# Kernel tuning notes

Measured on AMD Instinct MI355X. Metric: run time of the kernel, lower is better.

Reference implementation:

```python
import jax, jax.numpy as jnp
import numpy as np

B, C_IN, L = 1024, 3, 2048
D, K = 64, 8192          # embedding_dim, num_embeddings
BETA = 0.25
SLOPE = 0.001            # LeakyReLU negative slope


def _leaky(x):
    return jnp.where(x > 0, x, SLOPE * x)


def setup_inputs() -> dict:
    key = jax.random.key(0)
    ks = jax.random.split(key, 16)
    def lin(k, fan_in, shape):  # torch default conv init ~ U(-1/sqrt(fan_in), 1/sqrt(fan_in))
        b = 1.0 / np.sqrt(fan_in)
        return jax.random.uniform(k, shape, jnp.float32, -b, b)
    inp = {
        "x":  jax.random.normal(ks[0], (B, C_IN, L), jnp.float32),
        # encoder conv1x1 weights stored as [out, in]
        "W1": lin(ks[1], C_IN, (64, C_IN)),  "b1": lin(ks[2], C_IN, (64,)),
        "W2": lin(ks[3], 64,   (128, 64)),   "b2": lin(ks[4], 64,  (128,)),
        "W3": lin(ks[5], 128,  (D, 128)),    "b3": lin(ks[6], 128, (D,)),
        # codebook init: uniform(-1/K, 1/K) as in the torch module
        "codebook": jax.random.uniform(ks[7], (K, D), jnp.float32, -1.0 / K, 1.0 / K),
        # decoder convtranspose1x1 weights stored as [in, out]
        "U1": lin(ks[8],  D,   (D, 128)),    "c1": lin(ks[9],  D,   (128,)),
        "U2": lin(ks[10], 128, (128, 64)),   "c2": lin(ks[11], 128, (64,)),
        "U3": lin(ks[12], 64,  (64, C_IN)),  "c3": lin(ks[13], 64,  (C_IN,)),
    }
    return inp


def reference(x, W1, b1, W2, b2, W3, b3, codebook, U1, c1, U2, c2, U3, c3):
    # ---- encoder: conv1x1 stack over [B, C, L] then global max pool ----
    h = _leaky(jnp.einsum('oc,bcl->bol', W1, x) + b1[None, :, None])   # [B,64,L]
    h = _leaky(jnp.einsum('oc,bcl->bol', W2, h) + b2[None, :, None])   # [B,128,L]
    h = jnp.einsum('oc,bcl->bol', W3, h) + b3[None, :, None]           # [B,D,L]
    z = jnp.max(h, axis=-1)                                            # [B,D]

    # ---- vector quantizer ----
    d = (jnp.sum(z * z, axis=1, keepdims=True)
         + jnp.sum(codebook * codebook, axis=1)
         - 2.0 * z @ codebook.T)                                       # [B,K]
    idx = jnp.argmin(d, axis=1)                                        # [B]
    z_q = codebook[idx]                                                # [B,D]
    sg = jax.lax.stop_gradient
    loss = jnp.mean((sg(z_q) - z) ** 2) + BETA * jnp.mean((z_q - sg(z)) ** 2)
    z_q_st = z + sg(z_q - z)                                           # straight-through

    # ---- decoder: convtranspose1x1 on length-1 sequence == dense layers ----
    g = _leaky(z_q_st @ U1 + c1)                                       # [B,128]
    g = _leaky(g @ U2 + c2)                                            # [B,64]
    x_recon = (g @ U3 + c3)[:, :, None]                                # [B,3,1]
    return x_recon, loss, z
```

## Files before the change

kernel.cpp:

```cpp
#include <hip/hip_runtime.h>
#include <hip/hip_bf16.h>

#define BB 1024
#define LL 2048
#define KK 8192

typedef _Float16 f16x8 __attribute__((ext_vector_type(8)));
typedef _Float16 f16x2 __attribute__((ext_vector_type(2)));
typedef float    f32x4 __attribute__((ext_vector_type(4)));

__device__ __forceinline__ float leakyf(float v){ return fmaxf(v, 0.001f*v); }

__global__ __launch_bounds__(256, 2) void encoder_mfma(
    const float* __restrict__ x,
    const float* __restrict__ W1, const float* __restrict__ b1,
    const float* __restrict__ W2, const float* __restrict__ b2,
    const float* __restrict__ W3, const float* __restrict__ b3,
    float* __restrict__ z_out, _Float16* __restrict__ zh_out)
{
    const int b    = blockIdx.x;
    const int t    = threadIdx.x;
    const int wave = t >> 6;
    const int lane = t & 63;
    const int col  = lane & 15;
    const int quad = lane >> 4;

    __shared__ __align__(16) _Float16 h2lds[4*16*136];
    __shared__ float red[4][64];

    f16x8 w2f[2][8];
    #pragma unroll
    for (int ks=0; ks<2; ks++){
        #pragma unroll
        for (int nt=0; nt<8; nt++){
            const float* p = W2 + (nt*16+col)*64 + quad*8 + 32*ks;
            f16x8 f;
            #pragma unroll
            for (int j=0;j<8;j++) f[j] = (_Float16)p[j];
            w2f[ks][nt] = f;
        }
    }
    f16x8 w3f[4][4];
    #pragma unroll
    for (int ks=0; ks<4; ks++){
        #pragma unroll
        for (int nt=0; nt<4; nt++){
            const float* p = W3 + (nt*16+col)*128 + quad*8 + 32*ks;
            f16x8 f;
            #pragma unroll
            for (int j=0;j<8;j++) f[j] = (_Float16)p[j];
            w3f[ks][nt] = f;
        }
    }
    f16x2 w1p[2][4][3];
    f16x2 b1p[2][4];
    #pragma unroll
    for (int ks=0; ks<2; ks++){
        #pragma unroll
        for (int j2=0; j2<4; j2++){
            int c0 = quad*8 + 2*j2 + 32*ks;
            #pragma unroll
            for (int i=0;i<3;i++){
                f16x2 w; w[0] = (_Float16)W1[c0*3+i]; w[1] = (_Float16)W1[(c0+1)*3+i];
                w1p[ks][j2][i] = w;
            }
            f16x2 bb; bb[0] = (_Float16)b1[c0]; bb[1] = (_Float16)b1[c0+1];
            b1p[ks][j2] = bb;
        }
    }
    float bb2[8];
    #pragma unroll
    for (int nt=0; nt<8; nt++) bb2[nt] = b2[nt*16+col];

    f32x4 hm[4];
    #pragma unroll
    for (int nt=0;nt<4;nt++){
        hm[nt][0] = -__builtin_inff(); hm[nt][1] = -__builtin_inff();
        hm[nt][2] = -__builtin_inff(); hm[nt][3] = -__builtin_inff();
    }

    const float* xb = x + (size_t)b*3*LL;
    const int wave_off = wave*16*136;
    const int pbase = wave*16 + col;

    float x0n = xb[pbase], x1n = xb[LL+pbase], x2n = xb[2*LL+pbase];

    #pragma unroll 1
    for (int it=0; it<LL/64; it++){
        const float x0 = x0n, x1 = x1n, x2 = x2n;
        {
            int itn = it+1 < 32 ? it+1 : 31;
            int pn = itn*64 + pbase;
            x0n = xb[pn]; x1n = xb[LL+pn]; x2n = xb[2*LL+pn];
        }
        f16x2 xh0; xh0[0] = (_Float16)x0; xh0[1] = xh0[0];
        f16x2 xh1; xh1[0] = (_Float16)x1; xh1[1] = xh1[0];
        f16x2 xh2; xh2[0] = (_Float16)x2; xh2[1] = xh2[0];

        f16x8 a2[2];
        #pragma unroll
        for (int ks=0; ks<2; ks++){
            f16x8 a;
            #pragma unroll
            for (int j2=0; j2<4; j2++){
                f16x2 v = b1p[ks][j2];
                v += w1p[ks][j2][0]*xh0;
                v += w1p[ks][j2][1]*xh1;
                v += w1p[ks][j2][2]*xh2;
                _Float16 e0 = v[0], e1 = v[1];
                e0 = (e0 > (_Float16)0) ? e0 : e0*(_Float16)0.001f;
                e1 = (e1 > (_Float16)0) ? e1 : e1*(_Float16)0.001f;
                a[2*j2]   = e0;
                a[2*j2+1] = e1;
            }
            a2[ks] = a;
        }

        #pragma unroll
        for (int ph=0; ph<2; ph++){
            f32x4 acc2[4];
            #pragma unroll
            for (int n=0; n<4; n++){
                float bb = bb2[ph*4+n];
                acc2[n][0]=bb; acc2[n][1]=bb; acc2[n][2]=bb; acc2[n][3]=bb;
            }
            #pragma unroll
            for (int n=0; n<4; n++){
                acc2[n] = __builtin_amdgcn_mfma_f32_16x16x32_f16(a2[0], w2f[0][ph*4+n], acc2[n], 0,0,0);
                acc2[n] = __builtin_amdgcn_mfma_f32_16x16x32_f16(a2[1], w2f[1][ph*4+n], acc2[n], 0,0,0);
            }
            #pragma unroll
            for (int n=0; n<4; n++){
                #pragma unroll
                for (int j=0; j<4; j++){
                    float v = leakyf(acc2[n][j]);
                    h2lds[wave_off + (quad*4+j)*136 + (ph*4+n)*16+col] = (_Float16)v;
                }
            }
        }

        f32x4 acc3[4];
        #pragma unroll
        for (int nt=0; nt<4; nt++){ acc3[nt][0]=0.f; acc3[nt][1]=0.f; acc3[nt][2]=0.f; acc3[nt][3]=0.f; }
        #pragma unroll
        for (int ks=0; ks<4; ks++){
            f16x8 a3 = *(const f16x8*)&h2lds[wave_off + col*136 + quad*8 + 32*ks];
            #pragma unroll
            for (int nt=0; nt<4; nt++)
                acc3[nt] = __builtin_amdgcn_mfma_f32_16x16x32_f16(a3, w3f[ks][nt], acc3[nt], 0,0,0);
        }
        #pragma unroll
        for (int nt=0; nt<4; nt++){
            hm[nt][0] = fmaxf(hm[nt][0], acc3[nt][0]);
            hm[nt][1] = fmaxf(hm[nt][1], acc3[nt][1]);
            hm[nt][2] = fmaxf(hm[nt][2], acc3[nt][2]);
            hm[nt][3] = fmaxf(hm[nt][3], acc3[nt][3]);
        }
    }

    #pragma unroll
    for (int nt=0; nt<4; nt++){
        float v = fmaxf(fmaxf(hm[nt][0], hm[nt][1]), fmaxf(hm[nt][2], hm[nt][3]));
        v = fmaxf(v, __shfl_xor(v, 16, 64));
        v = fmaxf(v, __shfl_xor(v, 32, 64));
        if (quad == 0) red[wave][nt*16 + col] = v;
    }
    __syncthreads();
    if (t < 64){
        float v = fmaxf(fmaxf(red[0][t], red[1][t]), fmaxf(red[2][t], red[3][t])) + b3[t];
        z_out[(size_t)b*64 + t] = v;
        zh_out[(size_t)b*64 + t] = (_Float16)v;
    }
}

__global__ __launch_bounds__(256, 4) void vq_prep(
    const float* __restrict__ cb, _Float16* __restrict__ cbh, float* __restrict__ cnorm)
{
    const int t = threadIdx.x;
    const int e = blockIdx.x*4 + (t>>6);
    const int d = t & 63;
    float v = cb[(size_t)e*64 + d];
    cbh[(size_t)e*64 + d] = (_Float16)v;
    float p = v*v;
    #pragma unroll
    for (int s=32;s>0;s>>=1) p += __shfl_xor(p, s, 64);
    if (d==0) cnorm[e] = p;
}

__global__ __launch_bounds__(256, 2) void vq_mfma(
    const _Float16* __restrict__ zh, const _Float16* __restrict__ cbh,
    const float* __restrict__ cnorm,
    float* __restrict__ pval, int* __restrict__ pidx)
{
    const int t    = threadIdx.x;
    const int wave = t >> 6;
    const int lane = t & 63;
    const int col  = lane & 15;
    const int quad = lane >> 4;
    const int rb   = blockIdx.x >> 5;
    const int ns   = blockIdx.x & 31;
    const int rowbase = rb*64 + wave*16;

    f16x8 az[2];
    az[0] = *(const f16x8*)&zh[(size_t)(rowbase+col)*64 + quad*8];
    az[1] = *(const f16x8*)&zh[(size_t)(rowbase+col)*64 + quad*8 + 32];

    float best[4] = {__builtin_inff(),__builtin_inff(),__builtin_inff(),__builtin_inff()};
    int   bidx[4] = {0,0,0,0};

    int e = ns*256;
    f16x8 bf0 = *(const f16x8*)&cbh[(size_t)(e+col)*64 + quad*8];
    f16x8 bf1 = *(const f16x8*)&cbh[(size_t)(e+col)*64 + quad*8 + 32];
    float cn  = cnorm[e+col];

    #pragma unroll 1
    for (int nt=0; nt<16; nt++){
        f16x8 c0 = bf0, c1 = bf1;
        float cnc = cn;
        int ec = e;
        if (nt < 15){
            e += 16;
            bf0 = *(const f16x8*)&cbh[(size_t)(e+col)*64 + quad*8];
            bf1 = *(const f16x8*)&cbh[(size_t)(e+col)*64 + quad*8 + 32];
            cn  = cnorm[e+col];
        }
        f32x4 acc; acc[0]=0.f; acc[1]=0.f; acc[2]=0.f; acc[3]=0.f;
        acc = __builtin_amdgcn_mfma_f32_16x16x32_f16(az[0], c0, acc, 0,0,0);
        acc = __builtin_amdgcn_mfma_f32_16x16x32_f16(az[1], c1, acc, 0,0,0);
        int myidx = ec + col;
        #pragma unroll
        for (int r=0; r<4; r++){
            float d = fmaf(-2.0f, acc[r], cnc);
            if (d < best[r]){ best[r] = d; bidx[r] = myidx; }
        }
    }

    #pragma unroll
    for (int r=0; r<4; r++){
        float v = best[r]; int i = bidx[r];
        #pragma unroll
        for (int s=1; s<16; s<<=1){
            float ov = __shfl_xor(v, s, 64);
            int   oi = __shfl_xor(i, s, 64);
            if (ov < v || (ov == v && oi < i)){ v = ov; i = oi; }
        }
        if (col == 0){
            int row = rowbase + quad*4 + r;
            pval[row*32 + ns] = v;
            pidx[row*32 + ns] = i;
        }
    }
}

__global__ __launch_bounds__(256, 4) void vq_merge(
    const float* __restrict__ pval, const int* __restrict__ pidx, int* __restrict__ idx_out)
{
    const int row = blockIdx.x*256 + threadIdx.x;
    float best = __builtin_inff(); int bi = 0;
    #pragma unroll 4
    for (int s=0; s<32; s++){
        float v = pval[row*32 + s]; int i = pidx[row*32 + s];
        if (v < best || (v == best && i < bi)){ best = v; bi = i; }
    }
    idx_out[row] = bi;
}

__global__ __launch_bounds__(128, 1) void decoder_kernel(
    const float* __restrict__ z, const int* __restrict__ idx,
    const float* __restrict__ cb,
    const float* __restrict__ U1, const float* __restrict__ c1,
    const float* __restrict__ U2, const float* __restrict__ c2,
    const float* __restrict__ U3, const float* __restrict__ c3,
    float* __restrict__ xrec, float* __restrict__ loss_part)
{
    const int b = blockIdx.x;
    const int t = threadIdx.x;
    __shared__ float zst[64];
    __shared__ float g1[128];
    __shared__ float g2[64];
    const int kk = idx[b];
    if (t < 64){
        float zv = z[(size_t)b*64 + t];
        float zq = cb[(size_t)kk*64 + t];
        float diff = zq - zv;
        zst[t] = zv + diff;
        float p = diff*diff;
        #pragma unroll
        for (int s=32;s>0;s>>=1) p += __shfl_xor(p, s, 64);
        if (t==0) loss_part[b] = p;
    }
    __syncthreads();
    {
        float v = c1[t];
        #pragma unroll
        for (int d=0; d<64; d++) v = fmaf(zst[d], U1[d*128+t], v);
        g1[t] = leakyf(v);
    }
    __syncthreads();
    if (t < 64){
        float v = c2[t];
        #pragma unroll
        for (int j=0;j<128;j++) v = fmaf(g1[j], U2[j*64+t], v);
        g2[t] = leakyf(v);
    }
    __syncthreads();
    if (t < 3){
        float v = c3[t];
        #pragma unroll
        for (int j=0;j<64;j++) v = fmaf(g2[j], U3[j*3+t], v);
        xrec[(size_t)b*3 + t] = v;
    }
}

__global__ __launch_bounds__(256, 1) void loss_kernel(
    const float* __restrict__ loss_part, float* __restrict__ out)
{
    const int t = threadIdx.x;
    float s = 0.f;
    for (int i=t;i<BB;i+=256) s += loss_part[i];
    #pragma unroll
    for (int sh=32;sh>0;sh>>=1) s += __shfl_xor(s, sh, 64);
    __shared__ float w[4];
    if ((t&63)==0) w[t>>6] = s;
    __syncthreads();
    if (t==0) out[0] = (w[0]+w[1]+w[2]+w[3]) * (1.25f / 65536.0f);
}

extern "C" void kernel_launch(void* const* d_in, const int* in_sizes, int n_in,
                              void* d_out, int out_size, void* d_ws, size_t ws_size,
                              hipStream_t stream)
{
    const float* x  = (const float*)d_in[0];
    const float* W1 = (const float*)d_in[1];
    const float* b1 = (const float*)d_in[2];
    const float* W2 = (const float*)d_in[3];
    const float* b2 = (const float*)d_in[4];
    const float* W3 = (const float*)d_in[5];
    const float* b3 = (const float*)d_in[6];
    const float* cb = (const float*)d_in[7];
    const float* U1 = (const float*)d_in[8];
    const float* c1 = (const float*)d_in[9];
    const float* U2 = (const float*)d_in[10];
    const float* c2 = (const float*)d_in[11];
    const float* U3 = (const float*)d_in[12];
    const float* c3 = (const float*)d_in[13];

    float* out  = (float*)d_out;
    float* xrec = out;
    float* loss = out + 3072;
    float* z    = out + 3073;

    char* ws = (char*)d_ws;
    int*      idx   = (int*)ws;
    float*    lp    = (float*)(ws + 4096);
    _Float16* zh    = (_Float16*)(ws + 8192);
    float*    cnorm = (float*)(ws + 139264);
    float*    pval  = (float*)(ws + 172032);
    int*      pidx  = (int*)(ws + 303104);
    _Float16* cbh   = (_Float16*)(ws + 434176);

    hipLaunchKernelGGL(encoder_mfma, dim3(BB), dim3(256), 0, stream,
                       x, W1, b1, W2, b2, W3, b3, z, zh);
    hipLaunchKernelGGL(vq_prep, dim3(KK/4), dim3(256), 0, stream, cb, cbh, cnorm);
    hipLaunchKernelGGL(vq_mfma, dim3(512), dim3(256), 0, stream, zh, cbh, cnorm, pval, pidx);
    hipLaunchKernelGGL(vq_merge, dim3(4), dim3(256), 0, stream, pval, pidx, idx);
    hipLaunchKernelGGL(decoder_kernel, dim3(BB), dim3(128), 0, stream,
                       z, idx, cb, U1, c1, U2, c2, U3, c3, xrec, lp);
    hipLaunchKernelGGL(loss_kernel, dim3(1), dim3(256), 0, stream, lp, loss);
}
```

Measured before the change: 247.6 us.

## Fuse VQ merge into decoder, pack-convert encoder epilogue, swizzle LDS, vectorize prep

The encoder's layer-2 epilogue now converts MFMA results to packed fp16 before applying the bias and LeakyReLU, and writes to LDS through an XOR swizzle to cut bank conflicts. The input-layer LeakyReLU uses a packed max instead of per-element selects. vq_prep loads float4 and stores packed half4 with a 16-lane reduction. The separate vq_merge kernel is removed and its argmin is folded into the decoder through a warp shuffle reduction, which saves one launch. Doing the bias and activation in fp16 changes rounding slightly, which could flip a near-tied argmin.

Measured after the change: 226.2 us. 1.09x faster.

```diff
diff --git a/kernel.cpp b/kernel.cpp
--- a/kernel.cpp
+++ b/kernel.cpp
@@ -6,10 +6,14 @@
 #define KK 8192
 
 typedef _Float16 f16x8 __attribute__((ext_vector_type(8)));
+typedef _Float16 f16x4 __attribute__((ext_vector_type(4)));
 typedef _Float16 f16x2 __attribute__((ext_vector_type(2)));
 typedef float    f32x4 __attribute__((ext_vector_type(4)));
 
 __device__ __forceinline__ float leakyf(float v){ return fmaxf(v, 0.001f*v); }
+__device__ __forceinline__ f16x2 pkrtz(float a, float b){
+    return __builtin_bit_cast(f16x2, __builtin_amdgcn_cvt_pkrtz(a, b));
+}
 
 __global__ __launch_bounds__(256, 2) void encoder_mfma(
     const float* __restrict__ x,
@@ -68,9 +72,15 @@
             b1p[ks][j2] = bb;
         }
     }
-    float bb2[8];
-    #pragma unroll
-    for (int nt=0; nt<8; nt++) bb2[nt] = b2[nt*16+col];
+    f16x2 b2p[8];
+    #pragma unroll
+    for (int nt=0; nt<8; nt++){
+        _Float16 bv = (_Float16)b2[nt*16+col];
+        f16x2 p; p[0]=bv; p[1]=bv; b2p[nt]=p;
+    }
+
+    f16x2 k001; k001[0] = (_Float16)0.001f; k001[1] = (_Float16)0.001f;
+    f32x4 zc; zc[0]=0.f; zc[1]=0.f; zc[2]=0.f; zc[3]=0.f;
 
     f32x4 hm[4];
     #pragma unroll
@@ -80,8 +90,9 @@
     }
 
     const float* xb = x + (size_t)b*3*LL;
-    const int wave_off = wave*16*136;
+    const int wave_off = wave*2176;
     const int pbase = wave*16 + col;
+    const int rswz  = (col >> 2) << 4;
 
     float x0n = xb[pbase], x1n = xb[LL+pbase], x2n = xb[2*LL+pbase];
 
@@ -107,54 +118,47 @@
                 v += w1p[ks][j2][0]*xh0;
                 v += w1p[ks][j2][1]*xh1;
                 v += w1p[ks][j2][2]*xh2;
-                _Float16 e0 = v[0], e1 = v[1];
-                e0 = (e0 > (_Float16)0) ? e0 : e0*(_Float16)0.001f;
-                e1 = (e1 > (_Float16)0) ? e1 : e1*(_Float16)0.001f;
-                a[2*j2]   = e0;
-                a[2*j2+1] = e1;
+                v = __builtin_elementwise_max(v, v*k001);
+                a[2*j2]   = v[0];
+                a[2*j2+1] = v[1];
             }
             a2[ks] = a;
         }
 
         #pragma unroll
         for (int ph=0; ph<2; ph++){
-            f32x4 acc2[4];
             #pragma unroll
             for (int n=0; n<4; n++){
-                float bb = bb2[ph*4+n];
-                acc2[n][0]=bb; acc2[n][1]=bb; acc2[n][2]=bb; acc2[n][3]=bb;
+                const int nt = ph*4 + n;
+                f32x4 acc = __builtin_amdgcn_mfma_f32_16x16x32_f16(a2[0], w2f[0][nt], zc, 0,0,0);
+                acc = __builtin_amdgcn_mfma_f32_16x16x32_f16(a2[1], w2f[1][nt], acc, 0,0,0);
+                f16x2 p01 = pkrtz(acc[0], acc[1]);
+                f16x2 p23 = pkrtz(acc[2], acc[3]);
+                p01 += b2p[nt];  p23 += b2p[nt];
+                p01 = __builtin_elementwise_max(p01, p01*k001);
+                p23 = __builtin_elementwise_max(p23, p23*k001);
+                _Float16* wp = &h2lds[wave_off + quad*4*136 + ((nt ^ quad)<<4) + col];
+                wp[0]     = p01[0];
+                wp[136]   = p01[1];
+                wp[272]   = p23[0];
+                wp[408]   = p23[1];
             }
-            #pragma unroll
-            for (int n=0; n<4; n++){
-                acc2[n] = __builtin_amdgcn_mfma_f32_16x16x32_f16(a2[0], w2f[0][ph*4+n], acc2[n], 0,0,0);
-                acc2[n] = __builtin_amdgcn_mfma_f32_16x16x32_f16(a2[1], w2f[1][ph*4+n], acc2[n], 0,0,0);
-            }
-            #pragma unroll
-            for (int n=0; n<4; n++){
-                #pragma unroll
-                for (int j=0; j<4; j++){
-                    float v = leakyf(acc2[n][j]);
-                    h2lds[wave_off + (quad*4+j)*136 + (ph*4+n)*16+col] = (_Float16)v;
-                }
-            }
-        }
-
-        f32x4 acc3[4];
-        #pragma unroll
-        for (int nt=0; nt<4; nt++){ acc3[nt][0]=0.f; acc3[nt][1]=0.f; acc3[nt][2]=0.f; acc3[nt][3]=0.f; }
-        #pragma unroll
-        for (int ks=0; ks<4; ks++){
-            f16x8 a3 = *(const f16x8*)&h2lds[wave_off + col*136 + quad*8 + 32*ks];
-            #pragma unroll
-            for (int nt=0; nt<4; nt++)
-                acc3[nt] = __builtin_amdgcn_mfma_f32_16x16x32_f16(a3, w3f[ks][nt], acc3[nt], 0,0,0);
-        }
+        }
+
+        f16x8 a30 = *(const f16x8*)&h2lds[wave_off + col*136 + (( 0 + quad*8) ^ rswz)];
+        f16x8 a31 = *(const f16x8*)&h2lds[wave_off + col*136 + ((32 + quad*8) ^ rswz)];
+        f16x8 a32 = *(const f16x8*)&h2lds[wave_off + col*136 + ((64 + quad*8) ^ rswz)];
+        f16x8 a33 = *(const f16x8*)&h2lds[wave_off + col*136 + ((96 + quad*8) ^ rswz)];
         #pragma unroll
         for (int nt=0; nt<4; nt++){
-            hm[nt][0] = fmaxf(hm[nt][0], acc3[nt][0]);
-            hm[nt][1] = fmaxf(hm[nt][1], acc3[nt][1]);
-            hm[nt][2] = fmaxf(hm[nt][2], acc3[nt][2]);
-            hm[nt][3] = fmaxf(hm[nt][3], acc3[nt][3]);
+            f32x4 acc = __builtin_amdgcn_mfma_f32_16x16x32_f16(a30, w3f[0][nt], zc, 0,0,0);
+            acc = __builtin_amdgcn_mfma_f32_16x16x32_f16(a31, w3f[1][nt], acc, 0,0,0);
+            acc = __builtin_amdgcn_mfma_f32_16x16x32_f16(a32, w3f[2][nt], acc, 0,0,0);
+            acc = __builtin_amdgcn_mfma_f32_16x16x32_f16(a33, w3f[3][nt], acc, 0,0,0);
+            hm[nt][0] = fmaxf(hm[nt][0], acc[0]);
+            hm[nt][1] = fmaxf(hm[nt][1], acc[1]);
+            hm[nt][2] = fmaxf(hm[nt][2], acc[2]);
+            hm[nt][3] = fmaxf(hm[nt][3], acc[3]);
         }
     }
 
@@ -173,18 +177,22 @@
     }
 }
 
-__global__ __launch_bounds__(256, 4) void vq_prep(
+__global__ __launch_bounds__(256, 2) void vq_prep(
     const float* __restrict__ cb, _Float16* __restrict__ cbh, float* __restrict__ cnorm)
 {
     const int t = threadIdx.x;
-    const int e = blockIdx.x*4 + (t>>6);
-    const int d = t & 63;
-    float v = cb[(size_t)e*64 + d];
-    cbh[(size_t)e*64 + d] = (_Float16)v;
-    float p = v*v;
-    #pragma unroll
-    for (int s=32;s>0;s>>=1) p += __shfl_xor(p, s, 64);
-    if (d==0) cnorm[e] = p;
+    const int wave = t >> 6, lane = t & 63;
+    const int e   = blockIdx.x*16 + wave*4 + (lane >> 4);
+    const int sub = lane & 15;
+    const float4 v = *(const float4*)(cb + (size_t)e*64 + sub*4);
+    f16x2 h0 = pkrtz(v.x, v.y);
+    f16x2 h1 = pkrtz(v.z, v.w);
+    f16x4 hv; hv[0]=h0[0]; hv[1]=h0[1]; hv[2]=h1[0]; hv[3]=h1[1];
+    *(f16x4*)(cbh + (size_t)e*64 + sub*4) = hv;
+    float d = v.x*v.x + v.y*v.y + v.z*v.z + v.w*v.w;
+    #pragma unroll
+    for (int s=1; s<16; s<<=1) d += __shfl_xor(d, s, 64);
+    if (sub == 0) cnorm[e] = d;
 }
 
 __global__ __launch_bounds__(256, 2) void vq_mfma(
@@ -252,21 +260,9 @@
     }
 }
 
-__global__ __launch_bounds__(256, 4) void vq_merge(
-    const float* __restrict__ pval, const int* __restrict__ pidx, int* __restrict__ idx_out)
-{
-    const int row = blockIdx.x*256 + threadIdx.x;
-    float best = __builtin_inff(); int bi = 0;
-    #pragma unroll 4
-    for (int s=0; s<32; s++){
-        float v = pval[row*32 + s]; int i = pidx[row*32 + s];
-        if (v < best || (v == best && i < bi)){ best = v; bi = i; }
-    }
-    idx_out[row] = bi;
-}
-
-__global__ __launch_bounds__(128, 1) void decoder_kernel(
-    const float* __restrict__ z, const int* __restrict__ idx,
+__global__ __launch_bounds__(128, 2) void decoder_kernel(
+    const float* __restrict__ z,
+    const float* __restrict__ pval, const int* __restrict__ pidx,
     const float* __restrict__ cb,
     const float* __restrict__ U1, const float* __restrict__ c1,
     const float* __restrict__ U2, const float* __restrict__ c2,
@@ -275,10 +271,22 @@
 {
     const int b = blockIdx.x;
     const int t = threadIdx.x;
+    __shared__ int kk_s;
     __shared__ float zst[64];
     __shared__ float g1[128];
     __shared__ float g2[64];
-    const int kk = idx[b];
+    if (t < 32){
+        float v = pval[b*32 + t]; int i = pidx[b*32 + t];
+        #pragma unroll
+        for (int s=1; s<32; s<<=1){
+            float ov = __shfl_xor(v, s, 32);
+            int   oi = __shfl_xor(i, s, 32);
+            if (ov < v || (ov == v && oi < i)){ v = ov; i = oi; }
+        }
+        if (t==0) kk_s = i;
+    }
+    __syncthreads();
+    const int kk = kk_s;
     if (t < 64){
         float zv = z[(size_t)b*64 + t];
         float zq = cb[(size_t)kk*64 + t];
@@ -351,20 +359,18 @@
     float* z    = out + 3073;
 
     char* ws = (char*)d_ws;
-    int*      idx   = (int*)ws;
-    float*    lp    = (float*)(ws + 4096);
-    _Float16* zh    = (_Float16*)(ws + 8192);
-    float*    cnorm = (float*)(ws + 139264);
-    float*    pval  = (float*)(ws + 172032);
-    int*      pidx  = (int*)(ws + 303104);
-    _Float16* cbh   = (_Float16*)(ws + 434176);
-
+    float*    lp    = (float*)ws;
+    _Float16* zh    = (_Float16*)(ws + 4096);
+    float*    cnorm = (float*)(ws + 135168);
+    float*    pval  = (float*)(ws + 167936);
+    int*      pidx  = (int*)(ws + 299008);
+    _Float16* cbh   = (_Float16*)(ws + 430080);
+
+    hipLaunchKernelGGL(vq_prep, dim3(512), dim3(256), 0, stream, cb, cbh, cnorm);
     hipLaunchKernelGGL(encoder_mfma, dim3(BB), dim3(256), 0, stream,
                        x, W1, b1, W2, b2, W3, b3, z, zh);
-    hipLaunchKernelGGL(vq_prep, dim3(KK/4), dim3(256), 0, stream, cb, cbh, cnorm);
     hipLaunchKernelGGL(vq_mfma, dim3(512), dim3(256), 0, stream, zh, cbh, cnorm, pval, pidx);
-    hipLaunchKernelGGL(vq_merge, dim3(4), dim3(256), 0, stream, pval, pidx, idx);
     hipLaunchKernelGGL(decoder_kernel, dim3(BB), dim3(128), 0, stream,
-                       z, idx, cb, U1, c1, U2, c2, U3, c3, xrec, lp);
+                       z, pval, pidx, cb, U1, c1, U2, c2, U3, c3, xrec, lp);
     hipLaunchKernelGGL(loss_kernel, dim3(1), dim3(256), 0, stream, lp, loss);
 }
```
